# Performance work log

Hardware: AMD Instinct MI355X
Metric: run time of the kernel (lower is better)

The kernel has to match this reference:

```python
import jax, jax.numpy as jnp
import numpy as np

B, N, H, G, WIN, MH = 8, 8192, 128, 16, 3, 16
EPS = 1e-8


def _edges(n, w):
    # local sequence edges: i -> j for j in [i-w, i+w], j != i, 0 <= j < n
    i = np.arange(n)
    off = np.concatenate([np.arange(-w, 0), np.arange(1, w + 1)])
    j = i[:, None] + off[None, :]
    m = (j >= 0) & (j < n)
    src = np.broadcast_to(i[:, None], j.shape)[m]
    dst = j[m]
    return jnp.asarray(src, jnp.int32), jnp.asarray(dst, jnp.int32)


def setup_inputs() -> dict:
    key = jax.random.key(0)
    ks = jax.random.split(key, 10)
    d = {}
    d['x_scalar'] = jax.random.normal(ks[0], (B, N, H), jnp.float32)
    d['vec'] = jax.random.normal(ks[1], (B, N, 3, H), jnp.float32)
    d['W_geom'] = jax.random.normal(ks[2], (H, G), jnp.float32) / np.sqrt(H).astype(np.float32)
    d['q_w1'] = jax.random.normal(ks[3], (2, MH), jnp.float32) * 0.5
    d['q_b1'] = jnp.zeros((MH,), jnp.float32)
    d['q_w2'] = jax.random.normal(ks[4], (MH, 1), jnp.float32) * 0.25
    d['q_b2'] = jnp.zeros((1,), jnp.float32)
    d['k_w1'] = jax.random.normal(ks[5], (2, MH), jnp.float32) * 0.5
    d['k_b1'] = jnp.zeros((MH,), jnp.float32)
    d['k_w2'] = jax.random.normal(ks[6], (MH, 1), jnp.float32) * 0.25
    d['k_b2'] = jnp.zeros((1,), jnp.float32)
    d['Wq'] = jax.random.normal(ks[7], (G, H), jnp.float32) / np.sqrt(G).astype(np.float32)
    d['bq'] = jnp.zeros((H,), jnp.float32)
    d['Wk'] = jax.random.normal(ks[8], (G, H), jnp.float32) / np.sqrt(G).astype(np.float32)
    d['bk'] = jnp.zeros((H,), jnp.float32)
    return d


def _mlp(f, w1, b1, w2, b2):
    # f: (B,E,G,2) -> (B,E,G)
    return (jax.nn.silu(f @ w1 + b1) @ w2 + b2)[..., 0]


def reference(x_scalar, vec, W_geom, q_w1, q_b1, q_w2, q_b2,
              k_w1, k_b1, k_w2, k_b2, Wq, bq, Wk, bk):
    b, n, h = x_scalar.shape
    src, dst = _edges(n, WIN)
    # project vectors into geometry subspace: (B,N,3,G)
    vec_geom = jnp.einsum('bnch,hg->bncg', vec, W_geom)
    v_i = vec_geom[:, src]          # (B,E,3,G)
    v_j = vec_geom[:, dst]
    b_ij = v_j - v_i
    norm_b = jnp.maximum(jnp.linalg.norm(b_ij, axis=2, keepdims=True), EPS)
    e_ij = b_ij / norm_b            # unit edge directions (B,E,3,G)
    # scatter-add edge directions back to source nodes: (B,N,3,G)
    u = jnp.zeros((b, n, 3, G), x_scalar.dtype).at[:, src].add(e_ij)
    u_i = u[:, src]
    u_j = u[:, dst]
    dot_ui_e = (u_i * e_ij).sum(axis=2)                       # (B,E,G)
    norm_ui = jnp.maximum(jnp.linalg.norm(u_i, axis=2), EPS)
    ang_ij = jnp.clip(dot_ui_e / norm_ui, -1.0, 1.0)
    u_i_perp = u_i - dot_ui_e[:, :, None, :] * e_ij
    dot_uj_e = (u_j * e_ij).sum(axis=2)
    u_j_perp = u_j - dot_uj_e[:, :, None, :] * e_ij
    dot_perp = (u_i_perp * u_j_perp).sum(axis=2)
    np_i = jnp.maximum(jnp.linalg.norm(u_i_perp, axis=2), EPS)
    np_j = jnp.maximum(jnp.linalg.norm(u_j_perp, axis=2), EPS)
    dih_cos = jnp.clip(dot_perp / jnp.maximum(np_i * np_j, EPS), -1.0, 1.0)
    feats = jnp.stack([ang_ij, dih_cos], axis=-1)             # (B,E,G,2)
    g_geom_q = _mlp(feats, q_w1, q_b1, q_w2, q_b2)            # (B,E,G)
    g_geom_k = _mlp(feats, k_w1, k_b1, k_w2, k_b2)
    g_q = jax.nn.sigmoid(g_geom_q @ Wq + bq)                  # (B,E,H)
    g_k = jax.nn.sigmoid(g_geom_k @ Wk + bk)
    s_j = x_scalar[:, dst]                                    # (B,E,H)
    q = jnp.zeros_like(x_scalar).at[:, src].add(g_q * s_j)
    k = jnp.zeros_like(x_scalar).at[:, src].add(g_k * s_j)
    return q, k
```

## Files before the change

kernel.cpp:

```cpp
#include <hip/hip_runtime.h>

constexpr int NB = 8;
constexpr int NN = 8192;
constexpr int NH = 128;
constexpr int NG = 16;
constexpr int NT = 36;
constexpr int NT1 = NT + 1;
constexpr float NLOG2E = -1.44269504088896f;

typedef short s16x8 __attribute__((ext_vector_type(8)));
typedef float f32x4 __attribute__((ext_vector_type(4)));

__device__ __forceinline__ float frcp(float x) { return __builtin_amdgcn_rcpf(x); }
__device__ __forceinline__ float frsq(float x) { return __builtin_amdgcn_rsqf(x); }
__device__ __forceinline__ float fexp2(float x) {
#if __has_builtin(__builtin_amdgcn_exp2f)
    return __builtin_amdgcn_exp2f(x);
#else
    return __expf(x * 0.69314718056f);
#endif
}
__device__ __forceinline__ float fsigmoid(float x) { return frcp(1.f + __expf(-x)); }
__device__ __forceinline__ float fsilu(float x) { return x * fsigmoid(x); }
__device__ __forceinline__ float fclamp1(float x) { return fminf(fmaxf(x, -1.f), 1.f); }

__device__ __forceinline__ unsigned short f2bf(float x) {
    unsigned u = __builtin_bit_cast(unsigned, x);
    return (unsigned short)((u + 0x7FFFu + ((u >> 16) & 1u)) >> 16);
}
__device__ __forceinline__ unsigned packh2(float a, float b) {
    unsigned short lo = __builtin_bit_cast(unsigned short, (__fp16)a);
    unsigned short hi = __builtin_bit_cast(unsigned short, (__fp16)b);
    return (unsigned)lo | ((unsigned)hi << 16);
}
__device__ __forceinline__ float h2lo(unsigned u) {
    return (float)__builtin_bit_cast(__fp16, (unsigned short)(u & 0xFFFFu));
}
__device__ __forceinline__ float h2hi(unsigned u) {
    return (float)__builtin_bit_cast(__fp16, (unsigned short)(u >> 16));
}

__global__ __launch_bounds__(256) void k_table(
    const float* __restrict__ qw1, const float* __restrict__ qb1,
    const float* __restrict__ qw2, const float* __restrict__ qb2,
    const float* __restrict__ kw1, const float* __restrict__ kb1,
    const float* __restrict__ kw2, const float* __restrict__ kb2,
    unsigned* __restrict__ T) {
    int idx = blockIdx.x * 256 + threadIdx.x;
    if (idx >= NT1 * NT1) return;
    int ia = idx / NT1, id = idx % NT1;
    float a = -1.f + (float)ia * (2.f / NT);
    float d = -1.f + (float)id * (2.f / NT);
    float fq = qb2[0], fk = kb2[0];
#pragma unroll
    for (int m = 0; m < 16; ++m) {
        float hq = fmaf(a, qw1[m], fmaf(d, qw1[16 + m], qb1[m]));
        float hk = fmaf(a, kw1[m], fmaf(d, kw1[16 + m], kb1[m]));
        fq = fmaf(fsilu(hq), qw2[m], fq);
        fk = fmaf(fsilu(hk), kw2[m], fk);
    }
    T[idx] = packh2(fq, fk);
}

__global__ __launch_bounds__(256) void k_vecgeom(const float* __restrict__ vec,
                                                 const float* __restrict__ Wg,
                                                 float* __restrict__ vg) {
    __shared__ float Wl[NH * NG];
    for (int t = threadIdx.x; t < NH * NG; t += 256) Wl[t] = Wg[t];
    __syncthreads();

    int idx = blockIdx.x * 256 + threadIdx.x;
    int gq = idx & 3;
    int rc = idx >> 2;
    const float4* vrow = reinterpret_cast<const float4*>(vec + rc * NH);
    float a0 = 0.f, a1 = 0.f, a2 = 0.f, a3 = 0.f;
#pragma unroll 8
    for (int h4 = 0; h4 < 32; ++h4) {
        float4 v = vrow[h4];
        int h = h4 * 4;
        float4 w0 = *reinterpret_cast<const float4*>(&Wl[(h + 0) * NG + gq * 4]);
        float4 w1 = *reinterpret_cast<const float4*>(&Wl[(h + 1) * NG + gq * 4]);
        float4 w2 = *reinterpret_cast<const float4*>(&Wl[(h + 2) * NG + gq * 4]);
        float4 w3 = *reinterpret_cast<const float4*>(&Wl[(h + 3) * NG + gq * 4]);
        a0 = fmaf(v.x, w0.x, a0); a1 = fmaf(v.x, w0.y, a1); a2 = fmaf(v.x, w0.z, a2); a3 = fmaf(v.x, w0.w, a3);
        a0 = fmaf(v.y, w1.x, a0); a1 = fmaf(v.y, w1.y, a1); a2 = fmaf(v.y, w1.z, a2); a3 = fmaf(v.y, w1.w, a3);
        a0 = fmaf(v.z, w2.x, a0); a1 = fmaf(v.z, w2.y, a1); a2 = fmaf(v.z, w2.z, a2); a3 = fmaf(v.z, w2.w, a3);
        a0 = fmaf(v.w, w3.x, a0); a1 = fmaf(v.w, w3.y, a1); a2 = fmaf(v.w, w3.z, a2); a3 = fmaf(v.w, w3.w, a3);
    }
    *reinterpret_cast<float4*>(vg + rc * NG + gq * 4) = make_float4(a0, a1, a2, a3);
}

__global__ __launch_bounds__(256) void k_u(const float* __restrict__ vg,
                                           float* __restrict__ u) {
    int idx = blockIdx.x * 256 + threadIdx.x;
    int g = idx & 15;
    int bn = idx >> 4;
    int n = bn & (NN - 1);
    int base_i = bn * 48 + g;
    float vi0 = vg[base_i], vi1 = vg[base_i + 16], vi2 = vg[base_i + 32];
    float a0 = 0.f, a1 = 0.f, a2 = 0.f;
#pragma unroll
    for (int e = 0; e < 6; ++e) {
        int off = (e < 3) ? (e - 3) : (e - 2);
        int j = n + off;
        if (j < 0 || j >= NN) continue;
        int base_j = base_i + off * 48;
        float d0 = vg[base_j] - vi0;
        float d1 = vg[base_j + 16] - vi1;
        float d2 = vg[base_j + 32] - vi2;
        float r = frsq(fmaxf(d0 * d0 + d1 * d1 + d2 * d2, 1e-16f));
        a0 = fmaf(d0, r, a0); a1 = fmaf(d1, r, a1); a2 = fmaf(d2, r, a2);
    }
    u[base_i] = a0; u[base_i + 16] = a1; u[base_i + 32] = a2;
}

__device__ __forceinline__ void edge_gates(
    int base_i, int base_j,
    float vi0, float vi1, float vi2,
    float ui0, float ui1, float ui2, float rnui,
    const float* __restrict__ vg, const float* __restrict__ u,
    const unsigned (&Ts)[NT1 * NT1], float& fq, float& fk) {
    float d0 = vg[base_j] - vi0;
    float d1 = vg[base_j + 16] - vi1;
    float d2 = vg[base_j + 32] - vi2;
    float rb = frsq(fmaxf(d0 * d0 + d1 * d1 + d2 * d2, 1e-16f));
    float e0 = d0 * rb, e1 = d1 * rb, e2 = d2 * rb;
    float uj0 = u[base_j], uj1 = u[base_j + 16], uj2 = u[base_j + 32];
    float die = ui0 * e0 + ui1 * e1 + ui2 * e2;
    float ang = fclamp1(die * rnui);
    float p0 = ui0 - die * e0, p1 = ui1 - die * e1, p2 = ui2 - die * e2;
    float dje = uj0 * e0 + uj1 * e1 + uj2 * e2;
    float q0 = uj0 - dje * e0, q1 = uj1 - dje * e1, q2 = uj2 - dje * e2;
    float dp = p0 * q0 + p1 * q1 + p2 * q2;
    float pp = fmaxf(p0 * p0 + p1 * p1 + p2 * p2, 1e-16f);
    float qq = fmaxf(q0 * q0 + q1 * q1 + q2 * q2, 1e-16f);
    float dih = fclamp1(dp * frsq(pp * qq));

    float af = fmaf(ang, (float)NT * 0.5f, (float)NT * 0.5f);
    float df_ = fmaf(dih, (float)NT * 0.5f, (float)NT * 0.5f);
    int ia = min((int)af, NT - 1);
    int id = min((int)df_, NT - 1);
    float fa = af - (float)ia;
    float fd = df_ - (float)id;
    const unsigned* t0 = &Ts[ia * NT1 + id];
    unsigned c00 = t0[0], c01 = t0[1], c10 = t0[NT1], c11 = t0[NT1 + 1];
    float l0q = fmaf(fd, h2lo(c01) - h2lo(c00), h2lo(c00));
    float h0q = fmaf(fd, h2lo(c11) - h2lo(c10), h2lo(c10));
    fq = fmaf(fa, h0q - l0q, l0q);
    float l0k = fmaf(fd, h2hi(c01) - h2hi(c00), h2hi(c00));
    float h0k = fmaf(fd, h2hi(c11) - h2hi(c10), h2hi(c10));
    fk = fmaf(fa, h0k - l0k, l0k);
}

template <bool INT>
__device__ __forceinline__ void phaseA(
    int bn0, int n0, int gh, int sub, int lane,
    const float* __restrict__ vg, const float* __restrict__ u,
    const unsigned (&Ts)[NT1 * NT1],
    unsigned short (&As)[2][2][6][16][16]) {
    int nl = lane >> 4, g = lane & 15;
#pragma unroll
    for (int i = 0; i < 2; ++i) {
        int nq = sub * 2 + i;
        int node = nq * 4 + nl;
        int bn = bn0 + node;
        int base_i = bn * 48 + g;
        float vi0 = vg[base_i], vi1 = vg[base_i + 16], vi2 = vg[base_i + 32];
        float ui0 = u[base_i],  ui1 = u[base_i + 16],  ui2 = u[base_i + 32];
        float rnui = frsq(fmaxf(ui0 * ui0 + ui1 * ui1 + ui2 * ui2, 1e-16f));
#pragma unroll
        for (int e = 0; e < 6; ++e) {
            int off = (e < 3) ? (e - 3) : (e - 2);
            bool valid = INT || ((unsigned)(n0 + node + off) < (unsigned)NN);
            float fq = 0.f, fk = 0.f;
            if (valid)
                edge_gates(base_i, base_i + off * 48, vi0, vi1, vi2,
                           ui0, ui1, ui2, rnui, vg, u, Ts, fq, fk);
            As[gh][0][e][node][g] = f2bf(fq);
            As[gh][1][e][node][g] = f2bf(fk);
        }
    }
}

template <bool INT>
__device__ __forceinline__ void phaseB(
    int bn0, int n0, int gh, int qk, int lane,
    const float* __restrict__ xs,
    const unsigned short (&As)[2][2][6][16][16],
    const s16x8 (&Wl)[2][8][32], const float (&bs)[2][NH],
    float* __restrict__ out) {
    int c = lane & 15, rg = lane >> 4;
    s16x8 afr[6];
    int aidx = c * 2 + rg;
#pragma unroll
    for (int e = 0; e < 6; ++e)
        afr[e] = (lane < 32)
            ? reinterpret_cast<const s16x8*>(&As[gh][qk][e][0][0])[aidx]
            : (s16x8)0;

#pragma unroll
    for (int ht = 0; ht < 8; ++ht) {
        float xr[10];
#pragma unroll
        for (int d = 0; d < 10; ++d) {
            if (INT) {
                xr[d] = xs[(size_t)(bn0 + rg * 4 + d - 3) * NH + ht * 16 + c];
            } else {
                int gidx = bn0 + rg * 4 + d - 3;
                gidx = min(max(gidx, 0), NB * NN - 1);
                xr[d] = xs[(size_t)gidx * NH + ht * 16 + c];
            }
        }
        s16x8 bfr = (lane < 32) ? Wl[qk][ht][lane] : (s16x8)0;
        float b = bs[qk][ht * 16 + c];
        f32x4 bias4 = {b, b, b, b};
        f32x4 acc = {0.f, 0.f, 0.f, 0.f};
#pragma unroll
        for (int e = 0; e < 6; ++e) {
            f32x4 cc = __builtin_amdgcn_mfma_f32_16x16x32_bf16(afr[e], bfr, bias4, 0, 0, 0);
            int off = (e < 3) ? (e - 3) : (e - 2);
#pragma unroll
            for (int r = 0; r < 4; ++r) {
                float pr = frcp(1.f + fexp2(cc[r]));
                if (!INT) {
                    int jn = n0 + rg * 4 + r + off;
                    pr = ((unsigned)jn < (unsigned)NN) ? pr : 0.f;
                }
                acc[r] = fmaf(pr, xr[r + off + 3], acc[r]);
            }
        }
        float* o = out + (size_t)(bn0 + rg * 4) * NH + ht * 16 + c;
#pragma unroll
        for (int r = 0; r < 4; ++r) o[r * NH] = acc[r];
    }
}

__global__ __launch_bounds__(256, 4) void k_main(
    const float* __restrict__ vg, const float* __restrict__ u,
    const float* __restrict__ xs, const unsigned* __restrict__ T,
    const float* __restrict__ Wq, const float* __restrict__ bq,
    const float* __restrict__ Wk, const float* __restrict__ bk,
    float* __restrict__ outq, float* __restrict__ outk) {
    __shared__ unsigned Ts[NT1 * NT1];
    __shared__ __align__(16) unsigned short As[2][2][6][16][16];
    __shared__ s16x8 Wl[2][8][32];
    __shared__ float bs[2][NH];

    int tid = threadIdx.x;
    for (int t = tid; t < NT1 * NT1; t += 256) Ts[t] = T[t];

    for (int slot = tid; slot < 2 * 8 * 32; slot += 256) {
        int lane_in = slot & 31;
        int frag = slot >> 5;
        int fqk = frag >> 3, fht = frag & 7;
        const float* W = fqk ? Wk : Wq;
        int k0 = (lane_in >> 4) * 8, fcol = lane_in & 15;
        s16x8 v;
#pragma unroll
        for (int i = 0; i < 8; ++i)
            v[i] = (short)f2bf(NLOG2E * W[(k0 + i) * NH + fht * 16 + fcol]);
        Wl[fqk][fht][lane_in] = v;
    }
    if (tid < NH) bs[0][tid] = NLOG2E * bq[tid];
    else bs[1][tid - NH] = NLOG2E * bk[tid - NH];

    int w = tid >> 6, lane = tid & 63;
    int gh = w >> 1, sub = w & 1;

    __syncthreads();

#pragma unroll
    for (int it = 0; it < 2; ++it) {
        int grp = it * 2048 + blockIdx.x * 2 + gh;
        int bn0 = grp * 16;
        int n0 = bn0 & (NN - 1);
        bool interior = (n0 != 0) && (n0 != NN - 16);

        if (interior) phaseA<true>(bn0, n0, gh, sub, lane, vg, u, Ts, As);
        else          phaseA<false>(bn0, n0, gh, sub, lane, vg, u, Ts, As);

        __syncthreads();

        float* out = sub ? outk : outq;
        if (interior) phaseB<true>(bn0, n0, gh, sub, lane, xs, As, Wl, bs, out);
        else          phaseB<false>(bn0, n0, gh, sub, lane, xs, As, Wl, bs, out);

        __syncthreads();
    }
}

extern "C" void kernel_launch(void* const* d_in, const int* in_sizes, int n_in,
                              void* d_out, int out_size, void* d_ws, size_t ws_size,
                              hipStream_t stream) {
    const float* xs   = (const float*)d_in[0];
    const float* vec  = (const float*)d_in[1];
    const float* Wg   = (const float*)d_in[2];
    const float* qw1  = (const float*)d_in[3];
    const float* qb1  = (const float*)d_in[4];
    const float* qw2  = (const float*)d_in[5];
    const float* qb2  = (const float*)d_in[6];
    const float* kw1  = (const float*)d_in[7];
    const float* kb1  = (const float*)d_in[8];
    const float* kw2  = (const float*)d_in[9];
    const float* kb2  = (const float*)d_in[10];
    const float* Wq   = (const float*)d_in[11];
    const float* bq   = (const float*)d_in[12];
    const float* Wk   = (const float*)d_in[13];
    const float* bk   = (const float*)d_in[14];

    size_t vg_f = (size_t)NB * NN * 48;
    float* vg = (float*)d_ws;
    float* u  = vg + vg_f;
    unsigned* T = (unsigned*)(u + vg_f);
    float* outq = (float*)d_out;
    float* outk = outq + (size_t)NB * NN * NH;

    k_table<<<dim3((NT1 * NT1 + 255) / 256), dim3(256), 0, stream>>>(
        qw1, qb1, qw2, qb2, kw1, kb1, kw2, kb2, T);
    k_vecgeom<<<dim3(3072), dim3(256), 0, stream>>>(vec, Wg, vg);
    k_u<<<dim3(4096), dim3(256), 0, stream>>>(vg, u);
    k_main<<<dim3(1024), dim3(256), 0, stream>>>(
        vg, u, xs, T, Wq, bq, Wk, bk, outq, outk);
}
```

Baseline: 79.74 us.

## Process one 16-node group per block and split phase B over q/k and column halves

Measured after the change: 220.6 us. +176.6%, slower.

```diff
diff --git a/kernel.cpp b/kernel.cpp
--- a/kernel.cpp
+++ b/kernel.cpp
@@ -154,52 +154,66 @@
 
 template <bool INT>
 __device__ __forceinline__ void phaseA(
-    int bn0, int n0, int gh, int sub, int lane,
+    int bn0, int n0, int w, int lane,
     const float* __restrict__ vg, const float* __restrict__ u,
     const unsigned (&Ts)[NT1 * NT1],
-    unsigned short (&As)[2][2][6][16][16]) {
+    unsigned short (&As)[2][6][16][16]) {
     int nl = lane >> 4, g = lane & 15;
-#pragma unroll
-    for (int i = 0; i < 2; ++i) {
-        int nq = sub * 2 + i;
-        int node = nq * 4 + nl;
-        int bn = bn0 + node;
-        int base_i = bn * 48 + g;
-        float vi0 = vg[base_i], vi1 = vg[base_i + 16], vi2 = vg[base_i + 32];
-        float ui0 = u[base_i],  ui1 = u[base_i + 16],  ui2 = u[base_i + 32];
-        float rnui = frsq(fmaxf(ui0 * ui0 + ui1 * ui1 + ui2 * ui2, 1e-16f));
-#pragma unroll
-        for (int e = 0; e < 6; ++e) {
-            int off = (e < 3) ? (e - 3) : (e - 2);
-            bool valid = INT || ((unsigned)(n0 + node + off) < (unsigned)NN);
-            float fq = 0.f, fk = 0.f;
-            if (valid)
-                edge_gates(base_i, base_i + off * 48, vi0, vi1, vi2,
-                           ui0, ui1, ui2, rnui, vg, u, Ts, fq, fk);
-            As[gh][0][e][node][g] = f2bf(fq);
-            As[gh][1][e][node][g] = f2bf(fk);
-        }
+    int node = w * 4 + nl;
+    int bn = bn0 + node;
+    int base_i = bn * 48 + g;
+    float vi0 = vg[base_i], vi1 = vg[base_i + 16], vi2 = vg[base_i + 32];
+    float ui0 = u[base_i],  ui1 = u[base_i + 16],  ui2 = u[base_i + 32];
+    float rnui = frsq(fmaxf(ui0 * ui0 + ui1 * ui1 + ui2 * ui2, 1e-16f));
+#pragma unroll
+    for (int e = 0; e < 6; ++e) {
+        int off = (e < 3) ? (e - 3) : (e - 2);
+        bool valid = INT || ((unsigned)(n0 + node + off) < (unsigned)NN);
+        float fq = 0.f, fk = 0.f;
+        if (valid)
+            edge_gates(base_i, base_i + off * 48, vi0, vi1, vi2,
+                       ui0, ui1, ui2, rnui, vg, u, Ts, fq, fk);
+        As[0][e][node][g] = f2bf(fq);
+        As[1][e][node][g] = f2bf(fk);
     }
 }
 
 template <bool INT>
 __device__ __forceinline__ void phaseB(
-    int bn0, int n0, int gh, int qk, int lane,
+    int bn0, int n0, int qk, int hh, int lane,
     const float* __restrict__ xs,
-    const unsigned short (&As)[2][2][6][16][16],
-    const s16x8 (&Wl)[2][8][32], const float (&bs)[2][NH],
+    const float* __restrict__ W, const float* __restrict__ bias,
+    const unsigned short (&As)[2][6][16][16],
     float* __restrict__ out) {
     int c = lane & 15, rg = lane >> 4;
+
+    s16x8 bfr[4];
+    float bb[4];
+    int k0 = (lane >> 4) * 8;
+#pragma unroll
+    for (int t = 0; t < 4; ++t) {
+        int ht = hh * 4 + t;
+        s16x8 v = (s16x8)0;
+        if (lane < 32) {
+#pragma unroll
+            for (int i = 0; i < 8; ++i)
+                v[i] = (short)f2bf(NLOG2E * W[(k0 + i) * NH + ht * 16 + c]);
+        }
+        bfr[t] = v;
+        bb[t] = NLOG2E * bias[ht * 16 + c];
+    }
+
     s16x8 afr[6];
     int aidx = c * 2 + rg;
 #pragma unroll
     for (int e = 0; e < 6; ++e)
         afr[e] = (lane < 32)
-            ? reinterpret_cast<const s16x8*>(&As[gh][qk][e][0][0])[aidx]
+            ? reinterpret_cast<const s16x8*>(&As[qk][e][0][0])[aidx]
             : (s16x8)0;
 
 #pragma unroll
-    for (int ht = 0; ht < 8; ++ht) {
+    for (int t = 0; t < 4; ++t) {
+        int ht = hh * 4 + t;
         float xr[10];
 #pragma unroll
         for (int d = 0; d < 10; ++d) {
@@ -211,13 +225,11 @@
                 xr[d] = xs[(size_t)gidx * NH + ht * 16 + c];
             }
         }
-        s16x8 bfr = (lane < 32) ? Wl[qk][ht][lane] : (s16x8)0;
-        float b = bs[qk][ht * 16 + c];
-        f32x4 bias4 = {b, b, b, b};
+        f32x4 bias4 = {bb[t], bb[t], bb[t], bb[t]};
         f32x4 acc = {0.f, 0.f, 0.f, 0.f};
 #pragma unroll
         for (int e = 0; e < 6; ++e) {
-            f32x4 cc = __builtin_amdgcn_mfma_f32_16x16x32_bf16(afr[e], bfr, bias4, 0, 0, 0);
+            f32x4 cc = __builtin_amdgcn_mfma_f32_16x16x32_bf16(afr[e], bfr[t], bias4, 0, 0, 0);
             int off = (e < 3) ? (e - 3) : (e - 2);
 #pragma unroll
             for (int r = 0; r < 4; ++r) {
@@ -235,58 +247,37 @@
     }
 }
 
-__global__ __launch_bounds__(256, 4) void k_main(
+__global__ __launch_bounds__(256, 8) void k_main(
     const float* __restrict__ vg, const float* __restrict__ u,
     const float* __restrict__ xs, const unsigned* __restrict__ T,
     const float* __restrict__ Wq, const float* __restrict__ bq,
     const float* __restrict__ Wk, const float* __restrict__ bk,
     float* __restrict__ outq, float* __restrict__ outk) {
     __shared__ unsigned Ts[NT1 * NT1];
-    __shared__ __align__(16) unsigned short As[2][2][6][16][16];
-    __shared__ s16x8 Wl[2][8][32];
-    __shared__ float bs[2][NH];
+    __shared__ __align__(16) unsigned short As[2][6][16][16];
 
     int tid = threadIdx.x;
     for (int t = tid; t < NT1 * NT1; t += 256) Ts[t] = T[t];
 
-    for (int slot = tid; slot < 2 * 8 * 32; slot += 256) {
-        int lane_in = slot & 31;
-        int frag = slot >> 5;
-        int fqk = frag >> 3, fht = frag & 7;
-        const float* W = fqk ? Wk : Wq;
-        int k0 = (lane_in >> 4) * 8, fcol = lane_in & 15;
-        s16x8 v;
-#pragma unroll
-        for (int i = 0; i < 8; ++i)
-            v[i] = (short)f2bf(NLOG2E * W[(k0 + i) * NH + fht * 16 + fcol]);
-        Wl[fqk][fht][lane_in] = v;
-    }
-    if (tid < NH) bs[0][tid] = NLOG2E * bq[tid];
-    else bs[1][tid - NH] = NLOG2E * bk[tid - NH];
-
     int w = tid >> 6, lane = tid & 63;
-    int gh = w >> 1, sub = w & 1;
+    int grp = blockIdx.x;
+    int bn0 = grp * 16;
+    int n0 = bn0 & (NN - 1);
+    bool interior = (n0 != 0) && (n0 != NN - 16);
 
     __syncthreads();
 
-#pragma unroll
-    for (int it = 0; it < 2; ++it) {
-        int grp = it * 2048 + blockIdx.x * 2 + gh;
-        int bn0 = grp * 16;
-        int n0 = bn0 & (NN - 1);
-        bool interior = (n0 != 0) && (n0 != NN - 16);
-
-        if (interior) phaseA<true>(bn0, n0, gh, sub, lane, vg, u, Ts, As);
-        else          phaseA<false>(bn0, n0, gh, sub, lane, vg, u, Ts, As);
-
-        __syncthreads();
-
-        float* out = sub ? outk : outq;
-        if (interior) phaseB<true>(bn0, n0, gh, sub, lane, xs, As, Wl, bs, out);
-        else          phaseB<false>(bn0, n0, gh, sub, lane, xs, As, Wl, bs, out);
-
-        __syncthreads();
-    }
+    if (interior) phaseA<true>(bn0, n0, w, lane, vg, u, Ts, As);
+    else          phaseA<false>(bn0, n0, w, lane, vg, u, Ts, As);
+
+    __syncthreads();
+
+    int qk = w >> 1, hh = w & 1;
+    const float* W = qk ? Wk : Wq;
+    const float* bias = qk ? bk : bq;
+    float* out = qk ? outk : outq;
+    if (interior) phaseB<true>(bn0, n0, qk, hh, lane, xs, W, bias, As, out);
+    else          phaseB<false>(bn0, n0, qk, hh, lane, xs, W, bias, As, out);
 }
 
 extern "C" void kernel_launch(void* const* d_in, const int* in_sizes, int n_in,
@@ -319,6 +310,6 @@
         qw1, qb1, qw2, qb2, kw1, kb1, kw2, kb2, T);
     k_vecgeom<<<dim3(3072), dim3(256), 0, stream>>>(vec, Wg, vg);
     k_u<<<dim3(4096), dim3(256), 0, stream>>>(vg, u);
-    k_main<<<dim3(1024), dim3(256), 0, stream>>>(
+    k_main<<<dim3(4096), dim3(256), 0, stream>>>(
         vg, u, xs, T, Wq, bq, Wk, bk, outq, outk);
 }
```
